# Optimization experiments

Measured on AMD Instinct MI355X. Metric: run time of the kernel, lower is better.

Reference implementation:

```python
import jax, jax.numpy as jnp
import numpy as np

B, Hh, Ww, C = 4, 64, 64, 64


def setup_inputs() -> dict:
    key = jax.random.key(0)
    ks = jax.random.split(key, 5)
    scale = 1.0 / np.sqrt(C)
    return {
        "x": jax.random.normal(ks[0], (B, Hh, Ww, C), dtype=jnp.float32),
        "Wq": jax.random.normal(ks[1], (C, C), dtype=jnp.float32) * scale,
        "bq": jnp.zeros((C,), dtype=jnp.float32),
        "Wk": jax.random.normal(ks[2], (C, C), dtype=jnp.float32) * scale,
        "bk": jnp.zeros((C,), dtype=jnp.float32),
        "Wv": jax.random.normal(ks[3], (C, C), dtype=jnp.float32) * scale,
        "bv": jnp.zeros((C,), dtype=jnp.float32),
        "gamma": jax.random.normal(ks[4], (1,), dtype=jnp.float32) * 0.05,
    }


def reference(x, Wq, bq, Wk, bk, Wv, bv, gamma):
    b, h, w, c = x.shape
    n = h * w
    # 1x1 convs == per-pixel dense projections
    q = (jnp.einsum('bhwc,cf->bhwf', x, Wq) + bq).reshape(b, n, c)
    k = (jnp.einsum('bhwc,cf->bhwf', x, Wk) + bk).reshape(b, n, c)
    v = (jnp.einsum('bhwc,cf->bhwf', x, Wv) + bv).reshape(b, n, c)
    # energy[b, i, j] = <q_i, k_j>; no scaling, softmax over last axis (j)
    energy = jnp.einsum('bic,bjc->bij', q, k)
    attn = jax.nn.softmax(energy, axis=-1)
    # original: transpose(matmul(value^T, attention)) -> out[b,n,c] = sum_m attn[b,m,n] * v[b,m,c]
    out = jnp.einsum('bmn,bmc->bnc', attn, v)
    out = out.reshape(b, h, w, c)
    return gamma * out + x
```

## Files before the change

kernel.cpp:

```cpp
#include <hip/hip_runtime.h>
#include <hip/hip_bf16.h>


typedef __attribute__((ext_vector_type(8))) short short8;
typedef __attribute__((ext_vector_type(4))) short short4b;
typedef __attribute__((ext_vector_type(4))) float f32x4;
typedef __attribute__((ext_vector_type(4))) unsigned int u32x4;
typedef __attribute__((ext_vector_type(2))) unsigned int u32x2;

#define DEV static __device__ __forceinline__
#define LOG2E 1.4426950408889634f

DEV unsigned short f2bf(float f) {
    __hip_bfloat16 h = __float2bfloat16(f);
    return __builtin_bit_cast(unsigned short, h);
}
DEV unsigned int pack2(float lo, float hi) {
    return (unsigned int)f2bf(lo) | ((unsigned int)f2bf(hi) << 16);
}
DEV unsigned int pack2t(float lo, float hi) {
    unsigned int ul = __builtin_bit_cast(unsigned int, lo);
    unsigned int uh = __builtin_bit_cast(unsigned int, hi);
    return (uh & 0xffff0000u) | (ul >> 16);
}
DEV f32x4 MFMA32(short8 a, short8 b, f32x4 c) {
    return __builtin_amdgcn_mfma_f32_16x16x32_bf16(a, b, c, 0, 0, 0);
}
DEV f32x4 MFMA16(short4b a, short4b b, f32x4 c) {
#if __has_builtin(__builtin_amdgcn_mfma_f32_16x16x16_bf16)
    return __builtin_amdgcn_mfma_f32_16x16x16_bf16(a, b, c, 0, 0, 0);
#else
    return __builtin_amdgcn_mfma_f32_16x16x16bf16_1k(a, b, c, 0, 0, 0);
#endif
}
DEV float EXP2(float x) {
#if __has_builtin(__builtin_amdgcn_exp2f)
    return __builtin_amdgcn_exp2f(x);
#else
    return exp2f(x);
#endif
}

#define OFF_Q    0u
#define OFF_K    2097152u
#define OFF_VT   4194304u
#define OFF_WT   6291456u
#define OFF_S    6316032u
#define OFF_LR   6381568u

__global__ __launch_bounds__(256) void k0z(const float* __restrict__ Wq,
                                           const float* __restrict__ Wk,
                                           const float* __restrict__ Wv,
                                           unsigned short* __restrict__ wt,
                                           float* __restrict__ sbuf) {
    int e = blockIdx.x * 256 + threadIdx.x;
    sbuf[e] = 0.0f;
    if (e < 3 * 4096) {
        int w3 = e >> 12, rem = e & 4095, f = rem >> 6, c = rem & 63;
        const float* W = (w3 == 0) ? Wq : (w3 == 1) ? Wk : Wv;
        float s = (w3 == 0) ? LOG2E : 1.0f;
        wt[e] = f2bf(W[c * 64 + f] * s);
    }
}

__global__ __launch_bounds__(256) void k1_proj(const float* __restrict__ x,
                                               const unsigned short* __restrict__ wt,
                                               const float* __restrict__ bq,
                                               const float* __restrict__ bk,
                                               const float* __restrict__ bv,
                                               unsigned short* __restrict__ qf,
                                               unsigned short* __restrict__ kf,
                                               unsigned short* __restrict__ vf) {
    __shared__ __align__(16) char XT[8192];
    __shared__ __align__(16) char WT1[8192];
    __shared__ __align__(16) char OT[9216];
    int t = threadIdx.x, blk = blockIdx.x;
    int w3 = blk >> 8, rb = blk & 255;

    {
        int m = t >> 2, q4 = t & 3;
        const f32x4* xs = (const f32x4*)(x + (size_t)(rb * 64 + m) * 64 + q4 * 16);
        f32x4 fa = xs[0], f2 = xs[1], fc = xs[2], fd = xs[3];
        u32x4 u0 = { pack2(fa[0],fa[1]), pack2(fa[2],fa[3]), pack2(f2[0],f2[1]), pack2(f2[2],f2[3]) };
        u32x4 u1 = { pack2(fc[0],fc[1]), pack2(fc[2],fc[3]), pack2(fd[0],fd[1]), pack2(fd[2],fd[3]) };
        int sw = (m & 7) << 4;
        *(u32x4*)(XT + m * 128 + ((q4 * 32) ^ sw)) = u0;
        *(u32x4*)(XT + m * 128 + ((q4 * 32 + 16) ^ sw)) = u1;
    }
    {
        int f = t >> 2, q4 = t & 3;
        const u32x4* s = (const u32x4*)(wt + w3 * 4096 + f * 64 + q4 * 16);
        u32x4 u0 = s[0], u1 = s[1];
        int sw = (f & 7) << 4;
        *(u32x4*)(WT1 + f * 128 + ((q4 * 32) ^ sw)) = u0;
        *(u32x4*)(WT1 + f * 128 + ((q4 * 32 + 16) ^ sw)) = u1;
    }
    __syncthreads();

    int lane = t & 63, wid = t >> 6, g = lane >> 4, ln = lane & 15;
    int arow = wid * 16 + ln;
    short8 a0 = *(const short8*)(XT + arow * 128 + ((16 * g) ^ ((arow & 7) << 4)));
    short8 a1 = *(const short8*)(XT + arow * 128 + ((64 + 16 * g) ^ ((arow & 7) << 4)));
    const float* bias = (w3 == 0) ? bq : (w3 == 1) ? bk : bv;
    float bscale = (w3 == 0) ? LOG2E : 1.0f;

    unsigned short* ot = (unsigned short*)OT;
    #pragma unroll
    for (int fb = 0; fb < 4; ++fb) {
        int frow = fb * 16 + ln;
        short8 b0 = *(const short8*)(WT1 + frow * 128 + ((16 * g) ^ ((frow & 7) << 4)));
        short8 b1 = *(const short8*)(WT1 + frow * 128 + ((64 + 16 * g) ^ ((frow & 7) << 4)));
        f32x4 acc = {0.f, 0.f, 0.f, 0.f};
        acc = MFMA32(a0, b0, acc);
        acc = MFMA32(a1, b1, acc);
        float bval = bias[frow] * bscale;
        int mloc = wid * 16 + 4 * g;
        if (w3 < 2) {
            #pragma unroll
            for (int r = 0; r < 4; ++r)
                ot[(mloc + r) * 72 + frow] = f2bf(acc[r] + bval);
        } else {
            #pragma unroll
            for (int r = 0; r < 4; ++r)
                ot[frow * 72 + mloc + r] = f2bf(acc[r] + bval);
        }
    }
    __syncthreads();

    int mt_l = t >> 6, l = t & 63;
    size_t gmt = (size_t)rb * 4 + mt_l;
    if (w3 < 2) {
        unsigned short* dst = ((w3 == 0) ? qf : kf) + gmt * 1024;
        #pragma unroll
        for (int h = 0; h < 2; ++h) {
            u32x4 val = *(const u32x4*)(ot + (mt_l * 16 + (l & 15)) * 72 + h * 32 + 8 * (l >> 4));
            *(u32x4*)(dst + h * 512 + l * 8) = val;
        }
    } else {
        unsigned short* dst = vf + gmt * 1024;
        #pragma unroll
        for (int ct = 0; ct < 4; ++ct) {
            u32x2 val = *(const u32x2*)(ot + (ct * 16 + (l & 15)) * 72 + mt_l * 16 + 4 * (l >> 4));
            *(u32x2*)(dst + ct * 256 + l * 4) = val;
        }
    }
}

__global__ __launch_bounds__(256, 4) void k2_rowsum(const unsigned short* __restrict__ qf,
                                                    const unsigned short* __restrict__ kf,
                                                    float* __restrict__ sbuf) {
    int t = threadIdx.x, blk = blockIdx.x;
    int b = blk >> 8, ns = (blk >> 6) & 3, mb = blk & 63;
    int lane = t & 63, wid = t >> 6, g = lane >> 4, ln = lane & 15;

    size_t mt_g = (size_t)b * 256 + mb * 4 + wid;
    short8 a0 = *(const short8*)(qf + mt_g * 1024 + lane * 8);
    short8 a1 = *(const short8*)(qf + mt_g * 1024 + 512 + lane * 8);

    const unsigned short* kfb = kf + ((size_t)b * 256 + ns * 64) * 1024 + lane * 8;
    short8 kA0 = *(const short8*)(kfb);
    short8 kA1 = *(const short8*)(kfb + 512);
    short8 kB0 = *(const short8*)(kfb + 1024);
    short8 kB1 = *(const short8*)(kfb + 1536);

    f32x4 z = {0.f, 0.f, 0.f, 0.f};
    float acc0 = 0.f, acc1 = 0.f, acc2 = 0.f, acc3 = 0.f;
    for (int it = 0; it < 32; ++it) {
        short8 nA0, nA1, nB0, nB1;
        if (it < 31) {
            const unsigned short* kp = kfb + (size_t)(2 * it + 2) * 1024;
            nA0 = *(const short8*)(kp);
            nA1 = *(const short8*)(kp + 512);
            nB0 = *(const short8*)(kp + 1024);
            nB1 = *(const short8*)(kp + 1536);
        }
        f32x4 eA = MFMA32(a1, kA1, MFMA32(a0, kA0, z));
        f32x4 eB = MFMA32(a1, kB1, MFMA32(a0, kB0, z));
        acc0 += EXP2(eA[0]); acc1 += EXP2(eA[1]);
        acc2 += EXP2(eA[2]); acc3 += EXP2(eA[3]);
        acc0 += EXP2(eB[0]); acc1 += EXP2(eB[1]);
        acc2 += EXP2(eB[2]); acc3 += EXP2(eB[3]);
        kA0 = nA0; kA1 = nA1; kB0 = nB0; kB1 = nB1;
    }
    #pragma unroll
    for (int msk = 1; msk < 16; msk <<= 1) {
        acc0 += __shfl_xor(acc0, msk);
        acc1 += __shfl_xor(acc1, msk);
        acc2 += __shfl_xor(acc2, msk);
        acc3 += __shfl_xor(acc3, msk);
    }
    if (ln == 0) {
        float* base = sbuf + b * 4096 + (mb * 4 + wid) * 16 + 4 * g;
        unsafeAtomicAdd(base + 0, acc0);
        unsafeAtomicAdd(base + 1, acc1);
        unsafeAtomicAdd(base + 2, acc2);
        unsafeAtomicAdd(base + 3, acc3);
    }
}

__global__ __launch_bounds__(256) void r2_init(const float* __restrict__ sbuf,
                                               float* __restrict__ lrbuf,
                                               const float* __restrict__ x,
                                               float* __restrict__ outp) {
    int tid = blockIdx.x * 256 + threadIdx.x;
    if (tid < 16384) lrbuf[tid] = -__log2f(sbuf[tid]);
    f32x4 v = *(const f32x4*)(x + 4 * (size_t)tid);
    *(f32x4*)(outp + 4 * (size_t)tid) = v;
}

__global__ __launch_bounds__(256, 4) void k3_out(const unsigned short* __restrict__ qf,
                                                 const unsigned short* __restrict__ kf,
                                                 const unsigned short* __restrict__ vf,
                                                 const float* __restrict__ lrbuf,
                                                 const float* __restrict__ gamma,
                                                 float* __restrict__ outp) {
    int t = threadIdx.x, blk = blockIdx.x;
    int b = blk >> 8, ms = (blk >> 6) & 3, nblk = blk & 63;
    int lane = t & 63, wid = t >> 6, g = lane >> 4, ln = lane & 15;

    size_t nt_g = (size_t)b * 256 + nblk * 4 + wid;
    short8 kb0 = *(const short8*)(kf + nt_g * 1024 + lane * 8);
    short8 kb1 = *(const short8*)(kf + nt_g * 1024 + 512 + lane * 8);

    size_t mtbase = (size_t)b * 256 + ms * 64;
    const unsigned short* qb = qf + mtbase * 1024 + lane * 8;
    const unsigned short* vb = vf + mtbase * 1024 + lane * 4;
    const float* lrb = lrbuf + b * 4096 + ms * 1024 + 4 * g;

    short8 aA0 = *(const short8*)(qb);
    short8 aA1 = *(const short8*)(qb + 512);
    short4b vA0 = *(const short4b*)(vb);
    short4b vA1 = *(const short4b*)(vb + 256);
    short4b vA2 = *(const short4b*)(vb + 512);
    short4b vA3 = *(const short4b*)(vb + 768);
    f32x4 lcA = *(const f32x4*)(lrb);
    short8 aB0 = *(const short8*)(qb + 1024);
    short8 aB1 = *(const short8*)(qb + 1536);
    short4b vB0 = *(const short4b*)(vb + 1024);
    short4b vB1 = *(const short4b*)(vb + 1280);
    short4b vB2 = *(const short4b*)(vb + 1536);
    short4b vB3 = *(const short4b*)(vb + 1792);
    f32x4 lcB = *(const f32x4*)(lrb + 16);

    f32x4 z = {0.f, 0.f, 0.f, 0.f};
    f32x4 oacc[4] = {z, z, z, z};

    for (int it = 0; it < 32; ++it) {
        short8 nA0, nA1, nB0, nB1;
        short4b wA0, wA1, wA2, wA3, wB0, wB1, wB2, wB3;
        f32x4 plA, plB;
        if (it < 31) {
            int mt2 = 2 * it + 2;
            const unsigned short* qp = qb + (size_t)mt2 * 1024;
            nA0 = *(const short8*)(qp);
            nA1 = *(const short8*)(qp + 512);
            nB0 = *(const short8*)(qp + 1024);
            nB1 = *(const short8*)(qp + 1536);
            const unsigned short* vp = vb + (size_t)mt2 * 1024;
            wA0 = *(const short4b*)(vp);
            wA1 = *(const short4b*)(vp + 256);
            wA2 = *(const short4b*)(vp + 512);
            wA3 = *(const short4b*)(vp + 768);
            wB0 = *(const short4b*)(vp + 1024);
            wB1 = *(const short4b*)(vp + 1280);
            wB2 = *(const short4b*)(vp + 1536);
            wB3 = *(const short4b*)(vp + 1792);
            plA = *(const f32x4*)(lrb + mt2 * 16);
            plB = *(const f32x4*)(lrb + mt2 * 16 + 16);
        }
        f32x4 eA = MFMA32(aA1, kb1, MFMA32(aA0, kb0, lcA));
        float pA0 = EXP2(eA[0]), pA1 = EXP2(eA[1]), pA2 = EXP2(eA[2]), pA3 = EXP2(eA[3]);
        u32x2 pwA = { pack2t(pA0, pA1), pack2t(pA2, pA3) };
        short4b paA = __builtin_bit_cast(short4b, pwA);
        f32x4 eB = MFMA32(aB1, kb1, MFMA32(aB0, kb0, lcB));
        float pB0 = EXP2(eB[0]), pB1 = EXP2(eB[1]), pB2 = EXP2(eB[2]), pB3 = EXP2(eB[3]);
        u32x2 pwB = { pack2t(pB0, pB1), pack2t(pB2, pB3) };
        short4b paB = __builtin_bit_cast(short4b, pwB);

        oacc[0] = MFMA16(paA, vA0, oacc[0]);
        oacc[1] = MFMA16(paA, vA1, oacc[1]);
        oacc[2] = MFMA16(paA, vA2, oacc[2]);
        oacc[3] = MFMA16(paA, vA3, oacc[3]);
        oacc[0] = MFMA16(paB, vB0, oacc[0]);
        oacc[1] = MFMA16(paB, vB1, oacc[1]);
        oacc[2] = MFMA16(paB, vB2, oacc[2]);
        oacc[3] = MFMA16(paB, vB3, oacc[3]);

        aA0 = nA0; aA1 = nA1; aB0 = nB0; aB1 = nB1;
        vA0 = wA0; vA1 = wA1; vA2 = wA2; vA3 = wA3;
        vB0 = wB0; vB1 = wB1; vB2 = wB2; vB3 = wB3;
        lcA = plA; lcB = plB;
    }

    float gm = gamma[0];
    int nr = b * 4096 + (nblk * 4 + wid) * 16 + 4 * g;
    #pragma unroll
    for (int ct = 0; ct < 4; ++ct) {
        #pragma unroll
        for (int r = 0; r < 4; ++r)
            unsafeAtomicAdd(outp + (size_t)(nr + r) * 64 + ct * 16 + ln, gm * oacc[ct][r]);
    }
}

extern "C" void kernel_launch(void* const* d_in, const int* in_sizes, int n_in,
                              void* d_out, int out_size, void* d_ws, size_t ws_size,
                              hipStream_t stream) {
    const float* x  = (const float*)d_in[0];
    const float* Wq = (const float*)d_in[1];
    const float* bq = (const float*)d_in[2];
    const float* Wk = (const float*)d_in[3];
    const float* bk = (const float*)d_in[4];
    const float* Wv = (const float*)d_in[5];
    const float* bv = (const float*)d_in[6];
    const float* gm = (const float*)d_in[7];
    char* ws = (char*)d_ws;
    float* outp = (float*)d_out;

    unsigned short* qf = (unsigned short*)(ws + OFF_Q);
    unsigned short* kf = (unsigned short*)(ws + OFF_K);
    unsigned short* vf = (unsigned short*)(ws + OFF_VT);
    unsigned short* wt = (unsigned short*)(ws + OFF_WT);
    float* sbuf        = (float*)(ws + OFF_S);
    float* lrbuf       = (float*)(ws + OFF_LR);

    k0z<<<64, 256, 0, stream>>>(Wq, Wk, Wv, wt, sbuf);
    k1_proj<<<768, 256, 0, stream>>>(x, wt, bq, bk, bv, qf, kf, vf);
    k2_rowsum<<<1024, 256, 0, stream>>>(qf, kf, sbuf);
    r2_init<<<1024, 256, 0, stream>>>(sbuf, lrbuf, x, outp);
    k3_out<<<1024, 256, 0, stream>>>(qf, kf, vf, lrbuf, gm, outp);
}
```

Baseline: 156.2 us.

## Stage shared K/Q/V tiles through LDS with async global_load_lds double buffering

In both the rowsum and output kernels, each wave used to load the same K (or Q/V/log-rowsum) tiles from global memory into registers on its own. These tiles are now cooperatively staged into double-buffered shared memory with async global-to-LDS loads, one slice per wave, and read back from LDS. The aim is to cut redundant global and L2 traffic, since all four waves in a block share the tiles, and to lower register pressure. In exchange it adds a block-wide __syncthreads every iteration and LDS read latency inside the MFMA loop.

```diff
diff --git a/kernel.cpp b/kernel.cpp
--- a/kernel.cpp
+++ b/kernel.cpp
@@ -39,6 +39,12 @@
 #else
     return exp2f(x);
 #endif
+}
+DEV void gld16(const void* g, void* l) {
+    __builtin_amdgcn_global_load_lds(
+        (const __attribute__((address_space(1))) unsigned int*)g,
+        (__attribute__((address_space(3))) unsigned int*)l,
+        16, 0, 0);
 }
 
 #define OFF_Q    0u
@@ -149,6 +155,7 @@
 __global__ __launch_bounds__(256, 4) void k2_rowsum(const unsigned short* __restrict__ qf,
                                                     const unsigned short* __restrict__ kf,
                                                     float* __restrict__ sbuf) {
+    __shared__ __align__(16) char KB[2][4096];
     int t = threadIdx.x, blk = blockIdx.x;
     int b = blk >> 8, ns = (blk >> 6) & 3, mb = blk & 63;
     int lane = t & 63, wid = t >> 6, g = lane >> 4, ln = lane & 15;
@@ -157,30 +164,31 @@
     short8 a0 = *(const short8*)(qf + mt_g * 1024 + lane * 8);
     short8 a1 = *(const short8*)(qf + mt_g * 1024 + 512 + lane * 8);
 
-    const unsigned short* kfb = kf + ((size_t)b * 256 + ns * 64) * 1024 + lane * 8;
-    short8 kA0 = *(const short8*)(kfb);
-    short8 kA1 = *(const short8*)(kfb + 512);
-    short8 kB0 = *(const short8*)(kfb + 1024);
-    short8 kB1 = *(const short8*)(kfb + 1536);
+    const char* kbytes = (const char*)(kf + ((size_t)b * 256 + ns * 64) * 1024);
+    #define K2STAGE(BUF, IT) \
+        gld16(kbytes + (size_t)(IT) * 4096 + wid * 1024 + lane * 16, KB[BUF] + wid * 1024)
+
+    K2STAGE(0, 0);
+    __syncthreads();
 
     f32x4 z = {0.f, 0.f, 0.f, 0.f};
     float acc0 = 0.f, acc1 = 0.f, acc2 = 0.f, acc3 = 0.f;
+    int buf = 0;
     for (int it = 0; it < 32; ++it) {
-        short8 nA0, nA1, nB0, nB1;
-        if (it < 31) {
-            const unsigned short* kp = kfb + (size_t)(2 * it + 2) * 1024;
-            nA0 = *(const short8*)(kp);
-            nA1 = *(const short8*)(kp + 512);
-            nB0 = *(const short8*)(kp + 1024);
-            nB1 = *(const short8*)(kp + 1536);
-        }
+        if (it < 31) K2STAGE(buf ^ 1, it + 1);
+        const char* kt = KB[buf];
+        short8 kA0 = *(const short8*)(kt + lane * 16);
+        short8 kA1 = *(const short8*)(kt + 1024 + lane * 16);
+        short8 kB0 = *(const short8*)(kt + 2048 + lane * 16);
+        short8 kB1 = *(const short8*)(kt + 3072 + lane * 16);
         f32x4 eA = MFMA32(a1, kA1, MFMA32(a0, kA0, z));
         f32x4 eB = MFMA32(a1, kB1, MFMA32(a0, kB0, z));
         acc0 += EXP2(eA[0]); acc1 += EXP2(eA[1]);
         acc2 += EXP2(eA[2]); acc3 += EXP2(eA[3]);
         acc0 += EXP2(eB[0]); acc1 += EXP2(eB[1]);
         acc2 += EXP2(eB[2]); acc3 += EXP2(eB[3]);
-        kA0 = nA0; kA1 = nA1; kB0 = nB0; kB1 = nB1;
+        __syncthreads();
+        buf ^= 1;
     }
     #pragma unroll
     for (int msk = 1; msk < 16; msk <<= 1) {
@@ -214,6 +222,8 @@
                                                  const float* __restrict__ lrbuf,
                                                  const float* __restrict__ gamma,
                                                  float* __restrict__ outp) {
+    __shared__ __align__(16) char QV[2][8192];
+    __shared__ __align__(16) char LRS[4096];
     int t = threadIdx.x, blk = blockIdx.x;
     int b = blk >> 8, ms = (blk >> 6) & 3, nblk = blk & 63;
     int lane = t & 63, wid = t >> 6, g = lane >> 4, ln = lane & 15;
@@ -223,51 +233,41 @@
     short8 kb1 = *(const short8*)(kf + nt_g * 1024 + 512 + lane * 8);
 
     size_t mtbase = (size_t)b * 256 + ms * 64;
-    const unsigned short* qb = qf + mtbase * 1024 + lane * 8;
-    const unsigned short* vb = vf + mtbase * 1024 + lane * 4;
-    const float* lrb = lrbuf + b * 4096 + ms * 1024 + 4 * g;
-
-    short8 aA0 = *(const short8*)(qb);
-    short8 aA1 = *(const short8*)(qb + 512);
-    short4b vA0 = *(const short4b*)(vb);
-    short4b vA1 = *(const short4b*)(vb + 256);
-    short4b vA2 = *(const short4b*)(vb + 512);
-    short4b vA3 = *(const short4b*)(vb + 768);
-    f32x4 lcA = *(const f32x4*)(lrb);
-    short8 aB0 = *(const short8*)(qb + 1024);
-    short8 aB1 = *(const short8*)(qb + 1536);
-    short4b vB0 = *(const short4b*)(vb + 1024);
-    short4b vB1 = *(const short4b*)(vb + 1280);
-    short4b vB2 = *(const short4b*)(vb + 1536);
-    short4b vB3 = *(const short4b*)(vb + 1792);
-    f32x4 lcB = *(const f32x4*)(lrb + 16);
+    const char* qbytes = (const char*)(qf + mtbase * 1024);
+    const char* vbytes = (const char*)(vf + mtbase * 1024);
+    const float* lrsrc = lrbuf + b * 4096 + ms * 1024;
+
+    gld16(lrsrc + wid * 256 + lane * 4, LRS + wid * 1024);
+    #define K3STAGE(BUF, IT)                                                      \
+        do {                                                                      \
+            int r0_ = 2 * wid, r1_ = 2 * wid + 1;                                 \
+            const char* s0_ = (r0_ < 4 ? qbytes + r0_ * 1024                      \
+                                       : vbytes + (r0_ - 4) * 1024)               \
+                              + (size_t)(IT) * 4096 + lane * 16;                  \
+            const char* s1_ = (r1_ < 4 ? qbytes + r1_ * 1024                      \
+                                       : vbytes + (r1_ - 4) * 1024)               \
+                              + (size_t)(IT) * 4096 + lane * 16;                  \
+            gld16(s0_, QV[BUF] + r0_ * 1024);                                     \
+            gld16(s1_, QV[BUF] + r1_ * 1024);                                     \
+        } while (0)
+
+    K3STAGE(0, 0);
+    __syncthreads();
 
     f32x4 z = {0.f, 0.f, 0.f, 0.f};
     f32x4 oacc[4] = {z, z, z, z};
-
+    int buf = 0;
     for (int it = 0; it < 32; ++it) {
-        short8 nA0, nA1, nB0, nB1;
-        short4b wA0, wA1, wA2, wA3, wB0, wB1, wB2, wB3;
-        f32x4 plA, plB;
-        if (it < 31) {
-            int mt2 = 2 * it + 2;
-            const unsigned short* qp = qb + (size_t)mt2 * 1024;
-            nA0 = *(const short8*)(qp);
-            nA1 = *(const short8*)(qp + 512);
-            nB0 = *(const short8*)(qp + 1024);
-            nB1 = *(const short8*)(qp + 1536);
-            const unsigned short* vp = vb + (size_t)mt2 * 1024;
-            wA0 = *(const short4b*)(vp);
-            wA1 = *(const short4b*)(vp + 256);
-            wA2 = *(const short4b*)(vp + 512);
-            wA3 = *(const short4b*)(vp + 768);
-            wB0 = *(const short4b*)(vp + 1024);
-            wB1 = *(const short4b*)(vp + 1280);
-            wB2 = *(const short4b*)(vp + 1536);
-            wB3 = *(const short4b*)(vp + 1792);
-            plA = *(const f32x4*)(lrb + mt2 * 16);
-            plB = *(const f32x4*)(lrb + mt2 * 16 + 16);
-        }
+        if (it < 31) K3STAGE(buf ^ 1, it + 1);
+        const char* qt = QV[buf];
+        const char* vt = QV[buf] + 4096;
+        f32x4 lcA = *(const f32x4*)(LRS + it * 128 + g * 16);
+        f32x4 lcB = *(const f32x4*)(LRS + it * 128 + 64 + g * 16);
+        short8 aA0 = *(const short8*)(qt + lane * 16);
+        short8 aA1 = *(const short8*)(qt + 1024 + lane * 16);
+        short8 aB0 = *(const short8*)(qt + 2048 + lane * 16);
+        short8 aB1 = *(const short8*)(qt + 3072 + lane * 16);
+
         f32x4 eA = MFMA32(aA1, kb1, MFMA32(aA0, kb0, lcA));
         float pA0 = EXP2(eA[0]), pA1 = EXP2(eA[1]), pA2 = EXP2(eA[2]), pA3 = EXP2(eA[3]);
         u32x2 pwA = { pack2t(pA0, pA1), pack2t(pA2, pA3) };
@@ -277,19 +277,15 @@
         u32x2 pwB = { pack2t(pB0, pB1), pack2t(pB2, pB3) };
         short4b paB = __builtin_bit_cast(short4b, pwB);
 
-        oacc[0] = MFMA16(paA, vA0, oacc[0]);
-        oacc[1] = MFMA16(paA, vA1, oacc[1]);
-        oacc[2] = MFMA16(paA, vA2, oacc[2]);
-        oacc[3] = MFMA16(paA, vA3, oacc[3]);
-        oacc[0] = MFMA16(paB, vB0, oacc[0]);
-        oacc[1] = MFMA16(paB, vB1, oacc[1]);
-        oacc[2] = MFMA16(paB, vB2, oacc[2]);
-        oacc[3] = MFMA16(paB, vB3, oacc[3]);
-
-        aA0 = nA0; aA1 = nA1; aB0 = nB0; aB1 = nB1;
-        vA0 = wA0; vA1 = wA1; vA2 = wA2; vA3 = wA3;
-        vB0 = wB0; vB1 = wB1; vB2 = wB2; vB3 = wB3;
-        lcA = plA; lcB = plB;
+        #pragma unroll
+        for (int ct = 0; ct < 4; ++ct) {
+            short4b vA = *(const short4b*)(vt + ct * 512 + lane * 8);
+            short4b vB = *(const short4b*)(vt + 2048 + ct * 512 + lane * 8);
+            oacc[ct] = MFMA16(paA, vA, oacc[ct]);
+            oacc[ct] = MFMA16(paB, vB, oacc[ct]);
+        }
+        __syncthreads();
+        buf ^= 1;
     }
 
     float gm = gamma[0];
```

Result: faster. 126.6 us (-19.0%).
